# Kernel optimization log

Hardware: AMD Instinct MI355X
Metric: run time of the kernel (lower is better)

## Reference

```python
import jax, jax.numpy as jnp
import numpy as np


def setup_inputs() -> dict:
    key = jax.random.key(0)
    k1, k2, k3, k4 = jax.random.split(key, 4)
    H = W = D = 192
    I = jax.random.normal(k1, (1, 1, H, W, D), dtype=jnp.float32)
    dx_t = jax.random.normal(k2, (1, H, W, D), dtype=jnp.float32)
    dy_t = jax.random.normal(k3, (1, H, W, D), dtype=jnp.float32)
    dz_t = jax.random.normal(k4, (1, H, W, D), dtype=jnp.float32)
    return {"I": I, "dx_t": dx_t, "dy_t": dy_t, "dz_t": dz_t}


def reference(I, dx_t, dy_t, dz_t):
    # Trilinear warp, faithful to the torch module (valid for batch=1).
    B, C, H, W, D = I.shape
    # Identity meshgrid: x varies along width (axis 1), y along height (axis 0),
    # z along depth (axis 2) -- matches the numpy construction in __init__.
    x_mesh = jnp.arange(W, dtype=jnp.float32)[None, :, None]
    y_mesh = jnp.arange(H, dtype=jnp.float32)[:, None, None]
    z_mesh = jnp.arange(D, dtype=jnp.float32)[None, None, :]
    # +1 accounts for the zero-padding of I by 1 voxel on every side.
    x = dx_t[0] + x_mesh + 1.0  # [H,W,D]
    y = dy_t[0] + y_mesh + 1.0
    z = dz_t[0] + z_mesh + 1.0

    Ip = jnp.pad(I[0], ((0, 0), (1, 1), (1, 1), (1, 1)))  # [C,H+2,W+2,D+2]
    Hp, Wp, Dp = H + 2, W + 2, D + 2

    fx = jnp.floor(x).astype(jnp.int32)
    fy = jnp.floor(y).astype(jnp.int32)
    fz = jnp.floor(z).astype(jnp.int32)
    x0 = jnp.clip(fx, 0, Wp - 1); x1 = jnp.clip(fx + 1, 0, Wp - 1)
    y0 = jnp.clip(fy, 0, Hp - 1); y1 = jnp.clip(fy + 1, 0, Hp - 1)
    z0 = jnp.clip(fz, 0, Dp - 1); z1 = jnp.clip(fz + 1, 0, Dp - 1)

    # Fractional weights computed from the *clamped* upper corner (faithful).
    dx = x1.astype(jnp.float32) - x
    dy = y1.astype(jnp.float32) - y
    dz = z1.astype(jnp.float32) - z

    # Gather 8 corners: padded volume layout is [C, y, x, z].
    Ia = Ip[:, y0, x0, z0]
    Ib = Ip[:, y1, x0, z0]
    Ic = Ip[:, y0, x1, z0]
    Id = Ip[:, y1, x1, z0]
    Ie = Ip[:, y0, x0, z1]
    If = Ip[:, y1, x0, z1]
    Ig = Ip[:, y0, x1, z1]
    Ih = Ip[:, y1, x1, z1]

    wa = dz * dx * dy
    wb = dz * dx * (1 - dy)
    wc = dz * (1 - dx) * dy
    wd = dz * (1 - dx) * (1 - dy)
    we = (1 - dz) * dx * dy
    wf = (1 - dz) * dx * (1 - dy)
    wg = (1 - dz) * (1 - dx) * dy
    wh = (1 - dz) * (1 - dx) * (1 - dy)

    out = (wa * Ia + wb * Ib + wc * Ic + wd * Id
           + we * Ie + wf * If + wg * Ig + wh * Ih)  # [C,H,W,D]
    return out[None]  # [1,C,H,W,D]
```

## Files before the change

kernel.cpp:

```cpp
#include <hip/hip_runtime.h>

constexpr int H = 192, W = 192, D = 192;
constexpr int BH = 8, BW = 8, BZ = 16;
constexpr int TY = 16, TX = 16, TZ = 24;
constexpr int TILE_N = TY * TX * TZ;
constexpr int NCHUNK = TILE_N / 4;
constexpr int NINSTR = NCHUNK / 64;

__device__ __forceinline__ float ref_voxel(const float* __restrict__ I,
                                           float x, float y, float zf)
{
    int fx = (int)floorf(x), fy = (int)floorf(y), fz = (int)floorf(zf);
    int x0 = min(max(fx, 0), W + 1), x1 = min(max(fx + 1, 0), W + 1);
    int y0 = min(max(fy, 0), H + 1), y1 = min(max(fy + 1, 0), H + 1);
    int zp0 = min(max(fz, 0), D + 1), zp1 = min(max(fz + 1, 0), D + 1);
    float dx = (float)x1 - x, dy = (float)y1 - y, dz = (float)zp1 - zf;
    int xi0 = x0 - 1, xi1 = x1 - 1, yi0 = y0 - 1, yi1 = y1 - 1;
    int zi = zp0 - 1, zj = zp1 - 1;
    float ax0 = ((unsigned)xi0 < (unsigned)W) ? dx       : 0.f;
    float ax1 = ((unsigned)xi1 < (unsigned)W) ? 1.f - dx : 0.f;
    float ay0 = ((unsigned)yi0 < (unsigned)H) ? dy       : 0.f;
    float ay1 = ((unsigned)yi1 < (unsigned)H) ? 1.f - dy : 0.f;
    float az0 = ((unsigned)zi  < (unsigned)D) ? dz       : 0.f;
    float az1 = ((unsigned)zj  < (unsigned)D) ? 1.f - dz : 0.f;
    int xc0 = min(max(xi0, 0), W - 1), xc1 = min(max(xi1, 0), W - 1);
    int yc0 = min(max(yi0, 0), H - 1), yc1 = min(max(yi1, 0), H - 1);
    int zc0 = min(max(zi, 0), D - 1),  zc1 = min(max(zj, 0), D - 1);
    const float* r00 = I + (yc0 * W + xc0) * D;
    const float* r01 = I + (yc0 * W + xc1) * D;
    const float* r10 = I + (yc1 * W + xc0) * D;
    const float* r11 = I + (yc1 * W + xc1) * D;
    float s00 = az0 * r00[zc0] + az1 * r00[zc1];
    float s01 = az0 * r01[zc0] + az1 * r01[zc1];
    float s10 = az0 * r10[zc0] + az1 * r10[zc1];
    float s11 = az0 * r11[zc0] + az1 * r11[zc1];
    return ay0 * (ax0 * s00 + ax1 * s01) + ay1 * (ax0 * s10 + ax1 * s11);
}

__global__ __launch_bounds__(256, 8) void st_tile(
    const float* __restrict__ I,
    const float* __restrict__ dxt,
    const float* __restrict__ dyt,
    const float* __restrict__ dzt,
    float* __restrict__ out)
{
    __shared__ float tile[TILE_N];

    const int tid = threadIdx.x;
    const int bx = blockIdx.x, by = blockIdx.y, bz = blockIdx.z;
    const int w0 = bx * BW, h0 = by * BH, z0 = bz * BZ;
    const int xg0 = w0 - 4, yg0 = h0 - 4, zg0 = z0 - 4;

    {
        const unsigned wv = tid >> 6, lane = tid & 63;
        #pragma unroll
        for (unsigned t = 0; t < (unsigned)(NINSTR / 4); ++t) {
            unsigned i = wv + t * 4u;
            unsigned c = i * 64u + lane;
            unsigned row = c / 6u;
            unsigned s = c - row * 6u;
            unsigned ry = row >> 4, rx = row & 15u;
            int gy = min(max(yg0 + (int)ry, 0), H - 1);
            int gx = min(max(xg0 + (int)rx, 0), W - 1);
            int zs = min(max(zg0 + (int)(s * 4u), 0), D - 4);
            const float* src = I + ((gy * W + gx) * D + zs);
            __builtin_amdgcn_global_load_lds(
                (const __attribute__((address_space(1))) void*)src,
                (__attribute__((address_space(3))) void*)(tile + i * 256u),
                16, 0, 0);
        }
    }

    const int zq = tid & 3, wl = (tid >> 2) & 7, hl = tid >> 5;
    const int wg = w0 + wl, hg = h0 + hl;
    const int t4 = (hg * W + wg) * (D / 4) + (z0 >> 2) + zq;
    float4 vx = reinterpret_cast<const float4*>(dxt)[t4];
    float4 vy = reinterpret_cast<const float4*>(dyt)[t4];
    float4 vz = reinterpret_cast<const float4*>(dzt)[t4];

    asm volatile("s_waitcnt vmcnt(0)" ::: "memory");
    __syncthreads();

    float rxj[4] = {vx.x, vx.y, vx.z, vx.w};
    float ryj[4] = {vy.x, vy.y, vy.z, vy.w};
    float rzj[4] = {vz.x, vz.y, vz.z, vz.w};
    float ro[4];

    #pragma unroll
    for (int j = 0; j < 4; ++j) {
        const int zv = z0 + zq * 4 + j;
        float x  = rxj[j] + (float)(wg + 1);
        float y  = ryj[j] + (float)(hg + 1);
        float zf = rzj[j] + (float)(zv + 1);

        int fx = (int)floorf(x), fy = (int)floorf(y), fz = (int)floorf(zf);
        int x0 = min(max(fx, 0), W + 1), x1 = min(max(fx + 1, 0), W + 1);
        int y0 = min(max(fy, 0), H + 1), y1 = min(max(fy + 1, 0), H + 1);
        int zp0 = min(max(fz, 0), D + 1), zp1 = min(max(fz + 1, 0), D + 1);

        float dx = (float)x1 - x, dy = (float)y1 - y, dz = (float)zp1 - zf;

        int xi0 = x0 - 1, xi1 = x1 - 1, yi0 = y0 - 1, yi1 = y1 - 1;
        int zi = zp0 - 1, zj2 = zp1 - 1;

        float ax0 = ((unsigned)xi0 < (unsigned)W) ? dx       : 0.f;
        float ax1 = ((unsigned)xi1 < (unsigned)W) ? 1.f - dx : 0.f;
        float ay0 = ((unsigned)yi0 < (unsigned)H) ? dy       : 0.f;
        float ay1 = ((unsigned)yi1 < (unsigned)H) ? 1.f - dy : 0.f;
        float az0 = ((unsigned)zi  < (unsigned)D) ? dz       : 0.f;
        float az1 = ((unsigned)zj2 < (unsigned)D) ? 1.f - dz : 0.f;

        int xc0 = min(max(xi0, 0), W - 1), xc1 = min(max(xi1, 0), W - 1);
        int yc0 = min(max(yi0, 0), H - 1), yc1 = min(max(yi1, 0), H - 1);
        int zc  = min(max(zi, 0), D - 2);

        bool zlo = (zi <= D - 2);
        bool zhi = (zi >= 0);

        int lx0 = xc0 - xg0, lx1 = xc1 - xg0;
        int ly0 = yc0 - yg0, ly1 = yc1 - yg0;
        int lz  = zc - zg0;

        bool ok = ((unsigned)lx0 <= (unsigned)(TX - 1))
                & ((unsigned)lx1 <= (unsigned)(TX - 1))
                & ((unsigned)ly0 <= (unsigned)(TY - 1))
                & ((unsigned)ly1 <= (unsigned)(TY - 1))
                & ((unsigned)lz  <= (unsigned)(TZ - 2));

        int b00 = min(max((ly0 * TX + lx0) * TZ + lz, 0), TILE_N - 2);
        int b01 = min(max((ly0 * TX + lx1) * TZ + lz, 0), TILE_N - 2);
        int b10 = min(max((ly1 * TX + lx0) * TZ + lz, 0), TILE_N - 2);
        int b11 = min(max((ly1 * TX + lx1) * TZ + lz, 0), TILE_N - 2);

        float a0 = tile[b00], a1 = tile[b00 + 1];
        float b0 = tile[b01], b1 = tile[b01 + 1];
        float c0 = tile[b10], c1 = tile[b10 + 1];
        float d0 = tile[b11], d1 = tile[b11 + 1];

        float v000 = zlo ? a0 : a1, v001 = zhi ? a1 : a0;
        float v010 = zlo ? b0 : b1, v011 = zhi ? b1 : b0;
        float v100 = zlo ? c0 : c1, v101 = zhi ? c1 : c0;
        float v110 = zlo ? d0 : d1, v111 = zhi ? d1 : d0;
        float s00 = az0 * v000 + az1 * v001;
        float s01 = az0 * v010 + az1 * v011;
        float s10 = az0 * v100 + az1 * v101;
        float s11 = az0 * v110 + az1 * v111;
        float r = ay0 * (ax0 * s00 + ax1 * s01)
                + ay1 * (ax0 * s10 + ax1 * s11);

        ro[j] = __builtin_expect(ok, 1) ? r : ref_voxel(I, x, y, zf);
    }

    reinterpret_cast<float4*>(out)[t4] = make_float4(ro[0], ro[1], ro[2], ro[3]);
}

extern "C" void kernel_launch(void* const* d_in, const int* in_sizes, int n_in,
                              void* d_out, int out_size, void* d_ws, size_t ws_size,
                              hipStream_t stream) {
    const float* I   = (const float*)d_in[0];
    const float* dxt = (const float*)d_in[1];
    const float* dyt = (const float*)d_in[2];
    const float* dzt = (const float*)d_in[3];
    float* out = (float*)d_out;

    dim3 grid(W / BW, H / BH, D / BZ);
    hipLaunchKernelGGL(st_tile, grid, dim3(256), 0, stream,
                       I, dxt, dyt, dzt, out);
}
```

Baseline: 51.92 us.

## March blocks along z with double-buffered LDS slabs and interior fast path

Each block now walks six consecutive z-slabs, prefetching the next slab into a second LDS buffer together with the next displacement vectors while computing the current one. A wave-uniform interior check enables a simplified trilinear path using local floor coordinates, falling back to the original clamped logic otherwise. This aims to hide global load latency and cut per-voxel index arithmetic, at the cost of fewer blocks and lower occupancy (launch bounds 3, doubled LDS).

```diff
diff --git a/kernel.cpp b/kernel.cpp
--- a/kernel.cpp
+++ b/kernel.cpp
@@ -4,8 +4,8 @@
 constexpr int BH = 8, BW = 8, BZ = 16;
 constexpr int TY = 16, TX = 16, TZ = 24;
 constexpr int TILE_N = TY * TX * TZ;
-constexpr int NCHUNK = TILE_N / 4;
-constexpr int NINSTR = NCHUNK / 64;
+constexpr int KSTEPS = 6;
+constexpr int ZSPAN = BZ * KSTEPS;
 
 __device__ __forceinline__ float ref_voxel(const float* __restrict__ I,
                                            float x, float y, float zf)
@@ -37,121 +37,187 @@
     return ay0 * (ax0 * s00 + ax1 * s01) + ay1 * (ax0 * s10 + ax1 * s11);
 }
 
-__global__ __launch_bounds__(256, 8) void st_tile(
+__device__ __forceinline__ void stage_slab(const float* __restrict__ I,
+                                           float* dst, int xg0, int yg0, int zg0,
+                                           int tid)
+{
+    const unsigned wv = tid >> 6, lane = tid & 63;
+    #pragma unroll
+    for (unsigned t = 0; t < 6; ++t) {
+        unsigned i = wv + t * 4u;
+        unsigned c = i * 64u + lane;
+        unsigned rowc = c / 6u;
+        unsigned s = c - rowc * 6u;
+        unsigned ry = rowc >> 4, rx = rowc & 15u;
+        int gy = min(max(yg0 + (int)ry, 0), H - 1);
+        int gx = min(max(xg0 + (int)rx, 0), W - 1);
+        int zs = min(max(zg0 + (int)(s * 4u), 0), D - 4);
+        const float* src = I + ((gy * W + gx) * D + zs);
+        __builtin_amdgcn_global_load_lds(
+            (const __attribute__((address_space(1))) void*)src,
+            (__attribute__((address_space(3))) void*)(dst + i * 256u),
+            16, 0, 0);
+    }
+}
+
+__global__ __launch_bounds__(256, 3) void st_march(
     const float* __restrict__ I,
     const float* __restrict__ dxt,
     const float* __restrict__ dyt,
     const float* __restrict__ dzt,
     float* __restrict__ out)
 {
-    __shared__ float tile[TILE_N];
+    __shared__ __align__(16) float tile[2][TILE_N];
 
     const int tid = threadIdx.x;
-    const int bx = blockIdx.x, by = blockIdx.y, bz = blockIdx.z;
-    const int w0 = bx * BW, h0 = by * BH, z0 = bz * BZ;
-    const int xg0 = w0 - 4, yg0 = h0 - 4, zg0 = z0 - 4;
-
-    {
-        const unsigned wv = tid >> 6, lane = tid & 63;
-        #pragma unroll
-        for (unsigned t = 0; t < (unsigned)(NINSTR / 4); ++t) {
-            unsigned i = wv + t * 4u;
-            unsigned c = i * 64u + lane;
-            unsigned row = c / 6u;
-            unsigned s = c - row * 6u;
-            unsigned ry = row >> 4, rx = row & 15u;
-            int gy = min(max(yg0 + (int)ry, 0), H - 1);
-            int gx = min(max(xg0 + (int)rx, 0), W - 1);
-            int zs = min(max(zg0 + (int)(s * 4u), 0), D - 4);
-            const float* src = I + ((gy * W + gx) * D + zs);
-            __builtin_amdgcn_global_load_lds(
-                (const __attribute__((address_space(1))) void*)src,
-                (__attribute__((address_space(3))) void*)(tile + i * 256u),
-                16, 0, 0);
-        }
-    }
+    const int bx = blockIdx.x, by = blockIdx.y, bzc = blockIdx.z;
+    const int w0 = bx * BW, h0 = by * BH, zb = bzc * ZSPAN;
+    const int xg0 = w0 - 4, yg0 = h0 - 4;
 
     const int zq = tid & 3, wl = (tid >> 2) & 7, hl = tid >> 5;
     const int wg = w0 + wl, hg = h0 + hl;
-    const int t4 = (hg * W + wg) * (D / 4) + (z0 >> 2) + zq;
-    float4 vx = reinterpret_cast<const float4*>(dxt)[t4];
-    float4 vy = reinterpret_cast<const float4*>(dyt)[t4];
-    float4 vz = reinterpret_cast<const float4*>(dzt)[t4];
-
+    const int rowbase = (hg * W + wg) * (D / 4) + zq;
+
+    const int lox = max(0, -xg0),        hix = min(TX - 2, 190 - xg0);
+    const int loy = max(0, -yg0),        hiy = min(TY - 2, 190 - yg0);
+
+    stage_slab(I, tile[0], xg0, yg0, zb - 4, tid);
+    float4 cx = reinterpret_cast<const float4*>(dxt)[rowbase + (zb >> 2)];
+    float4 cy = reinterpret_cast<const float4*>(dyt)[rowbase + (zb >> 2)];
+    float4 cz = reinterpret_cast<const float4*>(dzt)[rowbase + (zb >> 2)];
     asm volatile("s_waitcnt vmcnt(0)" ::: "memory");
     __syncthreads();
 
-    float rxj[4] = {vx.x, vx.y, vx.z, vx.w};
-    float ryj[4] = {vy.x, vy.y, vy.z, vy.w};
-    float rzj[4] = {vz.x, vz.y, vz.z, vz.w};
-    float ro[4];
-
     #pragma unroll
-    for (int j = 0; j < 4; ++j) {
-        const int zv = z0 + zq * 4 + j;
-        float x  = rxj[j] + (float)(wg + 1);
-        float y  = ryj[j] + (float)(hg + 1);
-        float zf = rzj[j] + (float)(zv + 1);
-
-        int fx = (int)floorf(x), fy = (int)floorf(y), fz = (int)floorf(zf);
-        int x0 = min(max(fx, 0), W + 1), x1 = min(max(fx + 1, 0), W + 1);
-        int y0 = min(max(fy, 0), H + 1), y1 = min(max(fy + 1, 0), H + 1);
-        int zp0 = min(max(fz, 0), D + 1), zp1 = min(max(fz + 1, 0), D + 1);
-
-        float dx = (float)x1 - x, dy = (float)y1 - y, dz = (float)zp1 - zf;
-
-        int xi0 = x0 - 1, xi1 = x1 - 1, yi0 = y0 - 1, yi1 = y1 - 1;
-        int zi = zp0 - 1, zj2 = zp1 - 1;
-
-        float ax0 = ((unsigned)xi0 < (unsigned)W) ? dx       : 0.f;
-        float ax1 = ((unsigned)xi1 < (unsigned)W) ? 1.f - dx : 0.f;
-        float ay0 = ((unsigned)yi0 < (unsigned)H) ? dy       : 0.f;
-        float ay1 = ((unsigned)yi1 < (unsigned)H) ? 1.f - dy : 0.f;
-        float az0 = ((unsigned)zi  < (unsigned)D) ? dz       : 0.f;
-        float az1 = ((unsigned)zj2 < (unsigned)D) ? 1.f - dz : 0.f;
-
-        int xc0 = min(max(xi0, 0), W - 1), xc1 = min(max(xi1, 0), W - 1);
-        int yc0 = min(max(yi0, 0), H - 1), yc1 = min(max(yi1, 0), H - 1);
-        int zc  = min(max(zi, 0), D - 2);
-
-        bool zlo = (zi <= D - 2);
-        bool zhi = (zi >= 0);
-
-        int lx0 = xc0 - xg0, lx1 = xc1 - xg0;
-        int ly0 = yc0 - yg0, ly1 = yc1 - yg0;
-        int lz  = zc - zg0;
-
-        bool ok = ((unsigned)lx0 <= (unsigned)(TX - 1))
-                & ((unsigned)lx1 <= (unsigned)(TX - 1))
-                & ((unsigned)ly0 <= (unsigned)(TY - 1))
-                & ((unsigned)ly1 <= (unsigned)(TY - 1))
-                & ((unsigned)lz  <= (unsigned)(TZ - 2));
-
-        int b00 = min(max((ly0 * TX + lx0) * TZ + lz, 0), TILE_N - 2);
-        int b01 = min(max((ly0 * TX + lx1) * TZ + lz, 0), TILE_N - 2);
-        int b10 = min(max((ly1 * TX + lx0) * TZ + lz, 0), TILE_N - 2);
-        int b11 = min(max((ly1 * TX + lx1) * TZ + lz, 0), TILE_N - 2);
-
-        float a0 = tile[b00], a1 = tile[b00 + 1];
-        float b0 = tile[b01], b1 = tile[b01 + 1];
-        float c0 = tile[b10], c1 = tile[b10 + 1];
-        float d0 = tile[b11], d1 = tile[b11 + 1];
-
-        float v000 = zlo ? a0 : a1, v001 = zhi ? a1 : a0;
-        float v010 = zlo ? b0 : b1, v011 = zhi ? b1 : b0;
-        float v100 = zlo ? c0 : c1, v101 = zhi ? c1 : c0;
-        float v110 = zlo ? d0 : d1, v111 = zhi ? d1 : d0;
-        float s00 = az0 * v000 + az1 * v001;
-        float s01 = az0 * v010 + az1 * v011;
-        float s10 = az0 * v100 + az1 * v101;
-        float s11 = az0 * v110 + az1 * v111;
-        float r = ay0 * (ax0 * s00 + ax1 * s01)
-                + ay1 * (ax0 * s10 + ax1 * s11);
-
-        ro[j] = __builtin_expect(ok, 1) ? r : ref_voxel(I, x, y, zf);
+    for (int k = 0; k < KSTEPS; ++k) {
+        const int z0 = zb + k * BZ;
+        const int zg0 = z0 - 4;
+        const float* tl = tile[k & 1];
+
+        float4 nx, ny, nz;
+        if (k + 1 < KSTEPS) {
+            stage_slab(I, tile[(k + 1) & 1], xg0, yg0, z0 + BZ - 4, tid);
+            const int t4n = rowbase + ((z0 + BZ) >> 2);
+            nx = reinterpret_cast<const float4*>(dxt)[t4n];
+            ny = reinterpret_cast<const float4*>(dyt)[t4n];
+            nz = reinterpret_cast<const float4*>(dzt)[t4n];
+        }
+
+        const int lozk = max(0, -zg0), hizk = min(TZ - 2, 190 - zg0);
+
+        float rxj[4] = {cx.x, cx.y, cx.z, cx.w};
+        float ryj[4] = {cy.x, cy.y, cy.z, cy.w};
+        float rzj[4] = {cz.x, cz.y, cz.z, cz.w};
+        float ro[4];
+
+        int   lxa[4], lya[4], lza[4];
+        float txa[4], tya[4], tza[4];
+        bool  fa[4];
+        #pragma unroll
+        for (int j = 0; j < 4; ++j) {
+            float xl = rxj[j] + (float)(wl + 4);
+            float yl = ryj[j] + (float)(hl + 4);
+            float zl = rzj[j] + (float)(zq * 4 + j + 4);
+            float fxf = floorf(xl), fyf = floorf(yl), fzf = floorf(zl);
+            lxa[j] = (int)fxf; lya[j] = (int)fyf; lza[j] = (int)fzf;
+            txa[j] = xl - fxf; tya[j] = yl - fyf; tza[j] = zl - fzf;
+            fa[j] = ((unsigned)(lxa[j] - lox) <= (unsigned)(hix - lox))
+                  & ((unsigned)(lya[j] - loy) <= (unsigned)(hiy - loy))
+                  & ((unsigned)(lza[j] - lozk) <= (unsigned)(hizk - lozk));
+        }
+
+        if (__builtin_expect(__all(fa[0] & fa[1] & fa[2] & fa[3]), 1)) {
+            #pragma unroll
+            for (int j = 0; j < 4; ++j) {
+                int b = (lya[j] * TX + lxa[j]) * TZ + lza[j];
+                float a0 = tl[b],               a1 = tl[b + 1];
+                float b0 = tl[b + TZ],          b1 = tl[b + TZ + 1];
+                float c0 = tl[b + TX * TZ],     c1 = tl[b + TX * TZ + 1];
+                float d0 = tl[b + TX * TZ + TZ], d1 = tl[b + TX * TZ + TZ + 1];
+                float wz0 = 1.f - tza[j], wz1 = tza[j];
+                float wx0 = 1.f - txa[j], wx1 = txa[j];
+                float wy0 = 1.f - tya[j], wy1 = tya[j];
+                float s00 = wz0 * a0 + wz1 * a1;
+                float s01 = wz0 * b0 + wz1 * b1;
+                float s10 = wz0 * c0 + wz1 * c1;
+                float s11 = wz0 * d0 + wz1 * d1;
+                ro[j] = wy0 * (wx0 * s00 + wx1 * s01) + wy1 * (wx0 * s10 + wx1 * s11);
+            }
+        } else {
+            #pragma unroll
+            for (int j = 0; j < 4; ++j) {
+                const int zv = z0 + zq * 4 + j;
+                float x  = rxj[j] + (float)(wg + 1);
+                float y  = ryj[j] + (float)(hg + 1);
+                float zf = rzj[j] + (float)(zv + 1);
+
+                int fx = (int)floorf(x), fy = (int)floorf(y), fz = (int)floorf(zf);
+                int x0 = min(max(fx, 0), W + 1), x1 = min(max(fx + 1, 0), W + 1);
+                int y0 = min(max(fy, 0), H + 1), y1 = min(max(fy + 1, 0), H + 1);
+                int zp0 = min(max(fz, 0), D + 1), zp1 = min(max(fz + 1, 0), D + 1);
+
+                float dx = (float)x1 - x, dy = (float)y1 - y, dz = (float)zp1 - zf;
+
+                int xi0 = x0 - 1, xi1 = x1 - 1, yi0 = y0 - 1, yi1 = y1 - 1;
+                int zi = zp0 - 1, zj2 = zp1 - 1;
+
+                float ax0 = ((unsigned)xi0 < (unsigned)W) ? dx       : 0.f;
+                float ax1 = ((unsigned)xi1 < (unsigned)W) ? 1.f - dx : 0.f;
+                float ay0 = ((unsigned)yi0 < (unsigned)H) ? dy       : 0.f;
+                float ay1 = ((unsigned)yi1 < (unsigned)H) ? 1.f - dy : 0.f;
+                float az0 = ((unsigned)zi  < (unsigned)D) ? dz       : 0.f;
+                float az1 = ((unsigned)zj2 < (unsigned)D) ? 1.f - dz : 0.f;
+
+                int xc0 = min(max(xi0, 0), W - 1), xc1 = min(max(xi1, 0), W - 1);
+                int yc0 = min(max(yi0, 0), H - 1), yc1 = min(max(yi1, 0), H - 1);
+                int zc  = min(max(zi, 0), D - 2);
+
+                bool zlo = (zi <= D - 2);
+                bool zhi = (zi >= 0);
+
+                int lx0 = xc0 - xg0, lx1 = xc1 - xg0;
+                int ly0 = yc0 - yg0, ly1 = yc1 - yg0;
+                int lz  = zc - zg0;
+
+                bool ok = ((unsigned)lx0 <= (unsigned)(TX - 1))
+                        & ((unsigned)lx1 <= (unsigned)(TX - 1))
+                        & ((unsigned)ly0 <= (unsigned)(TY - 1))
+                        & ((unsigned)ly1 <= (unsigned)(TY - 1))
+                        & ((unsigned)lz  <= (unsigned)(TZ - 2));
+
+                int b00 = min(max((ly0 * TX + lx0) * TZ + lz, 0), TILE_N - 2);
+                int b01 = min(max((ly0 * TX + lx1) * TZ + lz, 0), TILE_N - 2);
+                int b10 = min(max((ly1 * TX + lx0) * TZ + lz, 0), TILE_N - 2);
+                int b11 = min(max((ly1 * TX + lx1) * TZ + lz, 0), TILE_N - 2);
+
+                float a0 = tl[b00], a1 = tl[b00 + 1];
+                float b0 = tl[b01], b1 = tl[b01 + 1];
+                float c0 = tl[b10], c1 = tl[b10 + 1];
+                float d0 = tl[b11], d1 = tl[b11 + 1];
+
+                float v000 = zlo ? a0 : a1, v001 = zhi ? a1 : a0;
+                float v010 = zlo ? b0 : b1, v011 = zhi ? b1 : b0;
+                float v100 = zlo ? c0 : c1, v101 = zhi ? c1 : c0;
+                float v110 = zlo ? d0 : d1, v111 = zhi ? d1 : d0;
+                float s00 = az0 * v000 + az1 * v001;
+                float s01 = az0 * v010 + az1 * v011;
+                float s10 = az0 * v100 + az1 * v101;
+                float s11 = az0 * v110 + az1 * v111;
+                float r = ay0 * (ax0 * s00 + ax1 * s01)
+                        + ay1 * (ax0 * s10 + ax1 * s11);
+
+                ro[j] = __builtin_expect(ok, 1) ? r : ref_voxel(I, x, y, zf);
+            }
+        }
+
+        reinterpret_cast<float4*>(out)[rowbase + (z0 >> 2)] =
+            make_float4(ro[0], ro[1], ro[2], ro[3]);
+
+        asm volatile("s_waitcnt vmcnt(0)" ::: "memory");
+        __syncthreads();
+
+        if (k + 1 < KSTEPS) { cx = nx; cy = ny; cz = nz; }
     }
-
-    reinterpret_cast<float4*>(out)[t4] = make_float4(ro[0], ro[1], ro[2], ro[3]);
 }
 
 extern "C" void kernel_launch(void* const* d_in, const int* in_sizes, int n_in,
@@ -163,7 +229,7 @@
     const float* dzt = (const float*)d_in[3];
     float* out = (float*)d_out;
 
-    dim3 grid(W / BW, H / BH, D / BZ);
-    hipLaunchKernelGGL(st_tile, grid, dim3(256), 0, stream,
+    dim3 grid(W / BW, H / BH, D / ZSPAN);
+    hipLaunchKernelGGL(st_march, grid, dim3(256), 0, stream,
                        I, dxt, dyt, dzt, out);
 }
```

New measurement: 55.22 us. +6.4%, slower.
